# Optimization experiments

Measured on AMD Instinct MI355X. Metric: run time of the kernel, lower is better.

Reference implementation:

```python
import jax, jax.numpy as jnp
import numpy as np

# 2D-LSTM wavefront recurrence (Bahar et al. 2018). Cell: gates i,f,o,lambda (sigmoid)
# and candidate g (tanh) from affine([x_cat; s_hor; s_ver]);
# c = f*(lam*c_hor + (1-lam)*c_ver) + i*g ; s = o*tanh(c).
# Returns full hidden-state grid states_s[1:,1:,:,:] reshaped to [I, O, B, H].

B, I, O, F, H = 64, 48, 48, 256, 256


def setup_inputs() -> dict:
    key = jax.random.key(0)
    k0, k1, k2, k3 = jax.random.split(key, 4)
    scale = 1.0 / np.sqrt(2 * F + 2 * H)
    return {
        "x": jax.random.normal(k0, (B, I, F), jnp.float32),
        "y": jax.random.normal(k1, (B, O, F), jnp.float32),
        "Wx": jax.random.normal(k2, (2 * F, 5 * H), jnp.float32) * scale,
        "Ws": jax.random.normal(k3, (2 * H, 5 * H), jnp.float32) * scale,
        "b": jnp.zeros((5 * H,), jnp.float32),
    }


def reference(x, y, Wx, Ws, b):
    Bn, In, Fn = x.shape
    On = y.shape[1]
    Hn = Ws.shape[0] // 2
    xT = jnp.transpose(x, (1, 0, 2))  # [I, B, F]
    yT = jnp.transpose(y, (1, 0, 2))  # [O, B, F]
    i_idx = jnp.arange(In)
    n_diag = In + On - 1

    def shift_down(a):  # lane i reads lane i-1 (zeros at i=0) -> horizontal predecessor
        return jnp.concatenate([jnp.zeros_like(a[:1]), a[:-1]], axis=0)

    def step(carry, d):
        s_buf, c_buf = carry  # [I, B, H]: states of diagonal d-1, keyed by input index i
        j = d - i_idx  # output index per lane on diagonal d
        valid = (j >= 0) & (j < On)
        s_hor, c_hor = shift_down(s_buf), shift_down(c_buf)  # cell (i-1, j)
        vmask = (j >= 1)[:, None, None]
        s_ver = jnp.where(vmask, s_buf, 0.0)  # cell (i, j-1)
        c_ver = jnp.where(vmask, c_buf, 0.0)
        y_cur = yT[jnp.clip(j, 0, On - 1)]  # [I, B, F]
        inp = jnp.concatenate([xT, y_cur], axis=-1)  # [I, B, 2F]
        st = jnp.concatenate([s_hor, s_ver], axis=-1)  # [I, B, 2H]
        pre = inp @ Wx + st @ Ws + b  # [I, B, 5H]
        ig, fg, og, lg, gg = jnp.split(pre, 5, axis=-1)
        ig, fg = jax.nn.sigmoid(ig), jax.nn.sigmoid(fg)
        og, lg = jax.nn.sigmoid(og), jax.nn.sigmoid(lg)
        gg = jnp.tanh(gg)
        c_next = fg * (lg * c_hor + (1.0 - lg) * c_ver) + ig * gg
        s_next = og * jnp.tanh(c_next)
        m = valid[:, None, None]
        s_new = jnp.where(m, s_next, 0.0)
        c_new = jnp.where(m, c_next, 0.0)
        return (s_new, c_new), s_new

    init = (jnp.zeros((In, Bn, Hn), x.dtype), jnp.zeros((In, Bn, Hn), x.dtype))
    _, ys = jax.lax.scan(step, init, jnp.arange(n_diag))  # [n_diag, I, B, H]
    ii = jnp.arange(In)[:, None]
    jj = jnp.arange(On)[None, :]
    grid = ys[ii + jj, ii]  # [I, O, B, H] : hidden state of every 2D cell
    return grid
```

## Files before the change

### kernel.cpp

```cpp
#include <hip/hip_runtime.h>
#include <hip/hip_bf16.h>

typedef __attribute__((ext_vector_type(8))) short short8;
typedef __attribute__((ext_vector_type(4))) float floatx4;

#define Bb 64
#define Ii 48
#define Oo 48
#define Ff 256
#define Hh 256
#define NG 1280
#define KK 512
#define CHUNK 80
#define NH 16
#define HCHUNKS 16
#define WORKERS 16
#define RING 4
#define WLDS_STRIDE 520
#define WLDS_STRIDE_PRE 264

__global__ __launch_bounds__(256) void pack_kernel(
    const float* __restrict__ Wx, const float* __restrict__ Ws,
    const float* __restrict__ x, const float* __restrict__ y,
    __hip_bfloat16* __restrict__ Wxp, __hip_bfloat16* __restrict__ Wsp,
    __hip_bfloat16* __restrict__ xb, __hip_bfloat16* __restrict__ yb) {
  int idx = blockIdx.x * blockDim.x + threadIdx.x;
  int stride = gridDim.x * blockDim.x;
  int total_w = NG * KK;
  for (int t = idx; t < total_w; t += stride) {
    int np = t / KK, k = t % KK;
    int hcp = np / CHUNK;
    int rem = np - hcp * CHUNK;
    int g = rem >> 4;
    int hsub = rem & 15;
    int orig = g * Hh + hcp * NH + hsub;
    Wxp[t] = __float2bfloat16(Wx[k * NG + orig]);
    Wsp[t] = __float2bfloat16(Ws[k * NG + orig]);
  }
  int total_x = Bb * Ii * Ff;
  for (int t = idx; t < total_x; t += stride) {
    int f = t % Ff; int rest = t / Ff; int b = rest % Bb; int i = rest / Bb;
    xb[(i * Bb + b) * Ff + f] = __float2bfloat16(x[(b * Ii + i) * Ff + f]);
    yb[(i * Bb + b) * Ff + f] = __float2bfloat16(y[(b * Oo + i) * Ff + f]);
  }
}

__global__ __launch_bounds__(256) void pregemm(
    const __hip_bfloat16* __restrict__ xb, const __hip_bfloat16* __restrict__ yb,
    const __hip_bfloat16* __restrict__ Wxp,
    float* __restrict__ Px, float* __restrict__ Py) {
  __shared__ __hip_bfloat16 Wl[CHUNK * WLDS_STRIDE_PRE];
  int wg = blockIdx.x;
  int isY = wg >= (Ii * HCHUNKS);
  int w = isY ? wg - Ii * HCHUNKS : wg;
  int mblk = w >> 4;
  int hc = w & 15;
  int n0 = hc * CHUNK;
  int koff = isY ? Ff : 0;
  int tid = threadIdx.x;
  for (int idx = tid; idx < CHUNK * (Ff / 8); idx += 256) {
    int cl = idx >> 5;
    int kb = (idx & 31) << 3;
    *(short8*)&Wl[cl * WLDS_STRIDE_PRE + kb] =
        *(const short8*)&Wxp[(n0 + cl) * KK + koff + kb];
  }
  __syncthreads();
  int wave = tid >> 6, lane = tid & 63;
  int lr = lane & 15, q = lane >> 4;
  const __hip_bfloat16* Arow = (isY ? yb : xb) + ((size_t)mblk * Bb + wave * 16 + lr) * Ff;
  floatx4 acc[5];
#pragma unroll
  for (int t = 0; t < 5; t++) acc[t] = (floatx4){0.f, 0.f, 0.f, 0.f};
#pragma unroll
  for (int ks = 0; ks < Ff / 32; ks++) {
    int k = ks * 32 + q * 8;
    short8 a = *(const short8*)(Arow + k);
#pragma unroll
    for (int t = 0; t < 5; t++) {
      short8 bfr = *(const short8*)&Wl[(t * 16 + lr) * WLDS_STRIDE_PRE + k];
      acc[t] = __builtin_amdgcn_mfma_f32_16x16x32_bf16(a, bfr, acc[t], 0, 0, 0);
    }
  }
  float* Pr = (isY ? Py : Px) + (size_t)mblk * Bb * NG + n0;
#pragma unroll
  for (int t = 0; t < 5; t++)
#pragma unroll
    for (int r = 0; r < 4; r++)
      Pr[(wave * 16 + q * 4 + r) * NG + t * 16 + lr] = acc[t][r];
}

__device__ __forceinline__ void wait16(const int* p) {
  while (__hip_atomic_load(p, __ATOMIC_RELAXED, __HIP_MEMORY_SCOPE_AGENT) < HCHUNKS)
    __builtin_amdgcn_s_sleep(1);
}

__device__ __forceinline__ short8 load8_sc(const __hip_bfloat16* p) {
  const unsigned long long* q = (const unsigned long long*)p;
  union { unsigned long long u[2]; short8 v; } r;
  r.u[0] = __hip_atomic_load(q,     __ATOMIC_RELAXED, __HIP_MEMORY_SCOPE_AGENT);
  r.u[1] = __hip_atomic_load(q + 1, __ATOMIC_RELAXED, __HIP_MEMORY_SCOPE_AGENT);
  return r.v;
}

__device__ __forceinline__ void store_bf16_sc(__hip_bfloat16* p, float f) {
  union { __hip_bfloat16 b; unsigned short u; } cv;
  cv.b = __float2bfloat16(f);
  __hip_atomic_store((unsigned short*)p, cv.u, __ATOMIC_RELAXED, __HIP_MEMORY_SCOPE_AGENT);
}

__global__ __launch_bounds__(256) void lstm_row(
    const float* __restrict__ Px, const float* __restrict__ Py,
    const float* __restrict__ bias, const __hip_bfloat16* __restrict__ Wsp,
    __hip_bfloat16* __restrict__ Sring, float* __restrict__ Cring,
    const __hip_bfloat16* __restrict__ Szero,
    float* __restrict__ out, int* __restrict__ done) {
  __shared__ __hip_bfloat16 Wl[CHUNK * WLDS_STRIDE];
  int wg = blockIdx.x;
  int worker = wg >> 4;
  int hc = wg & 15;
  int n0 = hc * CHUNK;
  int h0 = hc * NH;
  int tid = threadIdx.x;
  int wave = tid >> 6, lane = tid & 63;
  int lr = lane & 15, q = lane >> 4;
  const int brow = wave * 16 + q * 4;
  const int hme = h0 + lr;
  const size_t BH = (size_t)Bb * Hh;

  for (int idx = tid; idx < CHUNK * (KK / 8); idx += 256) {
    int cl = idx >> 6;
    int kb = (idx & 63) << 3;
    *(short8*)&Wl[cl * WLDS_STRIDE + kb] = *(const short8*)&Wsp[(n0 + cl) * KK + kb];
  }
  float bv[5];
#pragma unroll
  for (int g = 0; g < 5; g++) bv[g] = bias[g * Hh + hme];

#pragma unroll 1
  for (int rr = 0; rr < 3; rr++) {
    int i = worker + rr * WORKERS;
    float pxv[4][5];
#pragma unroll
    for (int ra = 0; ra < 4; ra++)
#pragma unroll
      for (int g = 0; g < 5; g++)
        pxv[ra][g] = Px[((size_t)i * Bb + (brow + ra)) * NG + n0 + g * 16 + lr];

    float cvreg[4];
#pragma unroll
    for (int it = 0; it < 4; it++) cvreg[it] = 0.f;

#pragma unroll 1
    for (int j = 0; j < Oo; j++) {
      const float* PyR = Py + (size_t)j * Bb * NG + n0;
      float pyv[4][5];
#pragma unroll
      for (int ra = 0; ra < 4; ra++)
#pragma unroll
        for (int g = 0; g < 5; g++)
          pyv[ra][g] = PyR[(size_t)(brow + ra) * NG + g * 16 + lr];

      if (tid < 3) {
        const int* fp = nullptr;
        if (tid == 0) {
          if (i > 0) fp = done + (i - 1) * Oo + j;
        } else if (tid == 1) {
          if (j > 0) fp = done + i * Oo + (j - 1);
        } else {
          if (i + 1 < Ii && j >= RING) fp = done + (i + 1) * Oo + (j - RING);
        }
        if (fp) wait16(fp);
      }
      __syncthreads();

      const __hip_bfloat16* Sv = (i > 0)
          ? Sring + ((size_t)(i - 1) * RING + (j & (RING - 1))) * BH : Szero;
      const __hip_bfloat16* Sh = (j > 0)
          ? Sring + ((size_t)i * RING + ((j - 1) & (RING - 1))) * BH : Szero;
      __hip_bfloat16* Sout = Sring + ((size_t)i * RING + (j & (RING - 1))) * BH;
      float* Cout = Cring + ((size_t)i * RING + (j & (RING - 1))) * BH;

      const __hip_bfloat16* SvR = Sv + (size_t)(wave * 16 + lr) * Hh;
      const __hip_bfloat16* ShR = Sh + (size_t)(wave * 16 + lr) * Hh;
      short8 av[16];
#pragma unroll
      for (int ks = 0; ks < 8; ks++)
        av[ks] = load8_sc(SvR + ks * 32 + q * 8);
#pragma unroll
      for (int ks = 0; ks < 8; ks++)
        av[8 + ks] = load8_sc(ShR + ks * 32 + q * 8);

      float chv[4];
      if (i > 0) {
        const float* Chp = Cring + ((size_t)(i - 1) * RING + (j & (RING - 1))) * BH;
#pragma unroll
        for (int ra = 0; ra < 4; ra++)
          chv[ra] = __hip_atomic_load(&Chp[(size_t)(brow + ra) * Hh + hme],
                                      __ATOMIC_RELAXED, __HIP_MEMORY_SCOPE_AGENT);
      } else {
#pragma unroll
        for (int ra = 0; ra < 4; ra++) chv[ra] = 0.f;
      }

      floatx4 acc[5];
#pragma unroll
      for (int t = 0; t < 5; t++) acc[t] = (floatx4){0.f, 0.f, 0.f, 0.f};
#pragma unroll
      for (int ks = 0; ks < KK / 32; ks++) {
        int k = ks * 32 + q * 8;
#pragma unroll
        for (int t = 0; t < 5; t++) {
          short8 bfr = *(const short8*)&Wl[(t * 16 + lr) * WLDS_STRIDE + k];
          acc[t] = __builtin_amdgcn_mfma_f32_16x16x32_bf16(av[ks], bfr, acc[t], 0, 0, 0);
        }
      }

      float snv[4];
#pragma unroll
      for (int ra = 0; ra < 4; ra++) {
        int b = brow + ra;
        float pre[5];
#pragma unroll
        for (int g = 0; g < 5; g++)
          pre[g] = acc[g][ra] + pxv[ra][g] + pyv[ra][g] + bv[g];
        float ig = 1.f / (1.f + __expf(-pre[0]));
        float fg = 1.f / (1.f + __expf(-pre[1]));
        float og = 1.f / (1.f + __expf(-pre[2]));
        float lg = 1.f / (1.f + __expf(-pre[3]));
        float gg = 1.f - 2.f / (__expf(2.f * pre[4]) + 1.f);
        float cn = fg * (lg * chv[ra] + (1.f - lg) * cvreg[ra]) + ig * gg;
        float tc = 1.f - 2.f / (__expf(2.f * cn) + 1.f);
        float sn = og * tc;
        cvreg[ra] = cn;
        snv[ra] = sn;
        __hip_atomic_store(&Cout[(size_t)b * Hh + hme], cn,
                           __ATOMIC_RELAXED, __HIP_MEMORY_SCOPE_AGENT);
        store_bf16_sc(&Sout[(size_t)b * Hh + hme], sn);
      }
      __syncthreads();
      if (tid == 0) atomicAdd(done + i * Oo + j, 1);
#pragma unroll
      for (int ra = 0; ra < 4; ra++)
        out[(((size_t)i * Oo + j) * Bb + (brow + ra)) * Hh + hme] = snv[ra];
    }
  }
}

extern "C" void kernel_launch(void* const* d_in, const int* in_sizes, int n_in,
                              void* d_out, int out_size, void* d_ws, size_t ws_size,
                              hipStream_t stream) {
  const float* x    = (const float*)d_in[0];
  const float* y    = (const float*)d_in[1];
  const float* Wx   = (const float*)d_in[2];
  const float* Ws   = (const float*)d_in[3];
  const float* bias = (const float*)d_in[4];
  float* out = (float*)d_out;

  char* ws = (char*)d_ws;
  size_t off = 0;
  auto alloc = [&](size_t bytes) -> void* {
    void* p = ws + off;
    off += (bytes + 255) & ~(size_t)255;
    return p;
  };
  __hip_bfloat16* Wxp = (__hip_bfloat16*)alloc((size_t)NG * KK * 2);
  __hip_bfloat16* Wsp = (__hip_bfloat16*)alloc((size_t)NG * KK * 2);
  __hip_bfloat16* xb  = (__hip_bfloat16*)alloc((size_t)Ii * Bb * Ff * 2);
  __hip_bfloat16* yb  = (__hip_bfloat16*)alloc((size_t)Oo * Bb * Ff * 2);
  float* Px = (float*)alloc((size_t)Ii * Bb * NG * 4);
  float* Py = (float*)alloc((size_t)Oo * Bb * NG * 4);
  __hip_bfloat16* Sring = (__hip_bfloat16*)alloc((size_t)Ii * RING * Bb * Hh * 2);
  float* Cring = (float*)alloc((size_t)Ii * RING * Bb * Hh * 4);
  char* zbase = ws + off;
  __hip_bfloat16* Szero = (__hip_bfloat16*)alloc((size_t)Bb * Hh * 2);
  int*   done = (int*)alloc((size_t)Ii * Oo * 4);
  size_t zBytes = (size_t)((ws + off) - zbase);

  hipMemsetAsync(zbase, 0, zBytes, stream);

  hipLaunchKernelGGL(pack_kernel, dim3(512), dim3(256), 0, stream,
                     Wx, Ws, x, y, Wxp, Wsp, xb, yb);
  hipLaunchKernelGGL(pregemm, dim3(2 * Ii * HCHUNKS), dim3(256), 0, stream,
                     xb, yb, Wxp, Px, Py);

  void* args[] = {(void*)&Px, (void*)&Py, (void*)&bias, (void*)&Wsp,
                  (void*)&Sring, (void*)&Cring, (void*)&Szero,
                  (void*)&out, (void*)&done};
  hipLaunchCooperativeKernel((void*)lstm_row, dim3(WORKERS * HCHUNKS), dim3(256),
                             args, 0, stream);
}
```

Baseline: 1.509 ms.

## Swizzle recurrent-weight LDS layout to fit two blocks per CU and widen workers

```diff
diff --git a/kernel.cpp b/kernel.cpp
--- a/kernel.cpp
+++ b/kernel.cpp
@@ -14,9 +14,7 @@
 #define CHUNK 80
 #define NH 16
 #define HCHUNKS 16
-#define WORKERS 16
 #define RING 4
-#define WLDS_STRIDE 520
 #define WLDS_STRIDE_PRE 264
 
 __global__ __launch_bounds__(256) void pack_kernel(
@@ -113,8 +111,10 @@
     const float* __restrict__ bias, const __hip_bfloat16* __restrict__ Wsp,
     __hip_bfloat16* __restrict__ Sring, float* __restrict__ Cring,
     const __hip_bfloat16* __restrict__ Szero,
-    float* __restrict__ out, int* __restrict__ done) {
-  __shared__ __hip_bfloat16 Wl[CHUNK * WLDS_STRIDE];
+    float* __restrict__ out, int* __restrict__ done,
+    int nworkers, int nrows) {
+  __shared__ __hip_bfloat16 Wl[CHUNK * KK];
+  char* Wb = (char*)Wl;
   int wg = blockIdx.x;
   int worker = wg >> 4;
   int hc = wg & 15;
@@ -129,16 +129,18 @@
 
   for (int idx = tid; idx < CHUNK * (KK / 8); idx += 256) {
     int cl = idx >> 6;
-    int kb = (idx & 63) << 3;
-    *(short8*)&Wl[cl * WLDS_STRIDE + kb] = *(const short8*)&Wsp[(n0 + cl) * KK + kb];
+    int boff = (idx & 63) << 4;
+    *(short8*)(Wb + cl * 1024 + (boff ^ ((cl & 7) << 4))) =
+        *(const short8*)&Wsp[(size_t)(n0 + cl) * KK + ((idx & 63) << 3)];
   }
   float bv[5];
 #pragma unroll
   for (int g = 0; g < 5; g++) bv[g] = bias[g * Hh + hme];
+  const int sw = (lr & 7) << 4;
 
 #pragma unroll 1
-  for (int rr = 0; rr < 3; rr++) {
-    int i = worker + rr * WORKERS;
+  for (int rr = 0; rr < nrows; rr++) {
+    int i = worker + rr * nworkers;
     float pxv[4][5];
 #pragma unroll
     for (int ra = 0; ra < 4; ra++)
@@ -207,10 +209,10 @@
       for (int t = 0; t < 5; t++) acc[t] = (floatx4){0.f, 0.f, 0.f, 0.f};
 #pragma unroll
       for (int ks = 0; ks < KK / 32; ks++) {
-        int k = ks * 32 + q * 8;
+        int boff = ks * 64 + q * 16;
 #pragma unroll
         for (int t = 0; t < 5; t++) {
-          short8 bfr = *(const short8*)&Wl[(t * 16 + lr) * WLDS_STRIDE + k];
+          short8 bfr = *(const short8*)(Wb + (t * 16 + lr) * 1024 + (boff ^ sw));
           acc[t] = __builtin_amdgcn_mfma_f32_16x16x32_bf16(av[ks], bfr, acc[t], 0, 0, 0);
         }
       }
@@ -283,9 +285,15 @@
   hipLaunchKernelGGL(pregemm, dim3(2 * Ii * HCHUNKS), dim3(256), 0, stream,
                      xb, yb, Wxp, Px, Py);
 
+  int perCU = 0;
+  int nworkers = 16, nrows = 3;
+  if (hipOccupancyMaxActiveBlocksPerMultiprocessor(&perCU, lstm_row, 256, 0)
+          == hipSuccess && perCU >= 2) {
+    nworkers = 24; nrows = 2;
+  }
   void* args[] = {(void*)&Px, (void*)&Py, (void*)&bias, (void*)&Wsp,
                   (void*)&Sring, (void*)&Cring, (void*)&Szero,
-                  (void*)&out, (void*)&done};
-  hipLaunchCooperativeKernel((void*)lstm_row, dim3(WORKERS * HCHUNKS), dim3(256),
+                  (void*)&out, (void*)&done, (void*)&nworkers, (void*)&nrows};
+  hipLaunchCooperativeKernel((void*)lstm_row, dim3(nworkers * HCHUNKS), dim3(256),
                              args, 0, stream);
 }
```

Result: no change. 1.507 ms (-0.1%).

## Use per-wave completion flags and XOR-swizzled LDS for recurrent weights

Applied to the files above, without the earlier changes.

```diff
diff --git a/kernel.cpp b/kernel.cpp
--- a/kernel.cpp
+++ b/kernel.cpp
@@ -16,7 +16,6 @@
 #define HCHUNKS 16
 #define WORKERS 16
 #define RING 4
-#define WLDS_STRIDE 520
 #define WLDS_STRIDE_PRE 264
 
 __global__ __launch_bounds__(256) void pack_kernel(
@@ -114,7 +113,8 @@
     __hip_bfloat16* __restrict__ Sring, float* __restrict__ Cring,
     const __hip_bfloat16* __restrict__ Szero,
     float* __restrict__ out, int* __restrict__ done) {
-  __shared__ __hip_bfloat16 Wl[CHUNK * WLDS_STRIDE];
+  __shared__ __hip_bfloat16 Wl[CHUNK * KK];
+  char* Wb = (char*)Wl;
   int wg = blockIdx.x;
   int worker = wg >> 4;
   int hc = wg & 15;
@@ -129,12 +129,16 @@
 
   for (int idx = tid; idx < CHUNK * (KK / 8); idx += 256) {
     int cl = idx >> 6;
-    int kb = (idx & 63) << 3;
-    *(short8*)&Wl[cl * WLDS_STRIDE + kb] = *(const short8*)&Wsp[(n0 + cl) * KK + kb];
+    int boff = (idx & 63) << 4;
+    *(short8*)(Wb + cl * 1024 + (boff ^ ((cl & 7) << 4))) =
+        *(const short8*)&Wsp[(size_t)(n0 + cl) * KK + ((idx & 63) << 3)];
   }
   float bv[5];
 #pragma unroll
   for (int g = 0; g < 5; g++) bv[g] = bias[g * Hh + hme];
+  const int sw = (lr & 7) << 4;
+
+  __syncthreads();
 
 #pragma unroll 1
   for (int rr = 0; rr < 3; rr++) {
@@ -160,18 +164,18 @@
         for (int g = 0; g < 5; g++)
           pyv[ra][g] = PyR[(size_t)(brow + ra) * NG + g * 16 + lr];
 
-      if (tid < 3) {
+      if (lane < 3) {
         const int* fp = nullptr;
-        if (tid == 0) {
-          if (i > 0) fp = done + (i - 1) * Oo + j;
-        } else if (tid == 1) {
-          if (j > 0) fp = done + i * Oo + (j - 1);
+        if (lane == 0) {
+          if (i > 0) fp = done + (((i - 1) * Oo + j) << 2) + wave;
+        } else if (lane == 1) {
+          if (j > 0) fp = done + ((i * Oo + (j - 1)) << 2) + wave;
         } else {
-          if (i + 1 < Ii && j >= RING) fp = done + (i + 1) * Oo + (j - RING);
+          if (i + 1 < Ii && j >= RING)
+            fp = done + (((i + 1) * Oo + (j - RING)) << 2) + wave;
         }
         if (fp) wait16(fp);
       }
-      __syncthreads();
 
       const __hip_bfloat16* Sv = (i > 0)
           ? Sring + ((size_t)(i - 1) * RING + (j & (RING - 1))) * BH : Szero;
@@ -207,10 +211,10 @@
       for (int t = 0; t < 5; t++) acc[t] = (floatx4){0.f, 0.f, 0.f, 0.f};
 #pragma unroll
       for (int ks = 0; ks < KK / 32; ks++) {
-        int k = ks * 32 + q * 8;
+        int boff = ks * 64 + q * 16;
 #pragma unroll
         for (int t = 0; t < 5; t++) {
-          short8 bfr = *(const short8*)&Wl[(t * 16 + lr) * WLDS_STRIDE + k];
+          short8 bfr = *(const short8*)(Wb + (t * 16 + lr) * 1024 + (boff ^ sw));
           acc[t] = __builtin_amdgcn_mfma_f32_16x16x32_bf16(av[ks], bfr, acc[t], 0, 0, 0);
         }
       }
@@ -237,8 +241,10 @@
                            __ATOMIC_RELAXED, __HIP_MEMORY_SCOPE_AGENT);
         store_bf16_sc(&Sout[(size_t)b * Hh + hme], sn);
       }
-      __syncthreads();
-      if (tid == 0) atomicAdd(done + i * Oo + j, 1);
+      asm volatile("s_waitcnt vmcnt(0)" ::: "memory");
+      if (lane == 0)
+        __hip_atomic_fetch_add(done + ((i * Oo + j) << 2) + wave, 1,
+                               __ATOMIC_RELAXED, __HIP_MEMORY_SCOPE_AGENT);
 #pragma unroll
       for (int ra = 0; ra < 4; ra++)
         out[(((size_t)i * Oo + j) * Bb + (brow + ra)) * Hh + hme] = snv[ra];
@@ -273,7 +279,7 @@
   float* Cring = (float*)alloc((size_t)Ii * RING * Bb * Hh * 4);
   char* zbase = ws + off;
   __hip_bfloat16* Szero = (__hip_bfloat16*)alloc((size_t)Bb * Hh * 2);
-  int*   done = (int*)alloc((size_t)Ii * Oo * 4);
+  int*   done = (int*)alloc((size_t)Ii * Oo * 4 * sizeof(int));
   size_t zBytes = (size_t)((ws + off) - zbase);
 
   hipMemsetAsync(zbase, 0, zBytes, stream);
```

Result: slower. 2.193 ms (+45.4%).
